# Performance work log

Hardware: AMD Instinct MI355X
Metric: run time of the kernel (lower is better)

## Reference

```python
import jax, jax.numpy as jnp
import numpy as np

A_LO, A_HI = -1.0, 1.0  # arbitrary_range


def _kbit_gaussian(q_lo: float, q_hi: float, n_bit: int) -> jnp.ndarray:
    # torch: norm.ppf of quantiles 1/n..(n-1)/n, cast to fp16, then affine-normalize in fp16
    p = jnp.arange(1, n_bit, dtype=jnp.float32) / n_bit
    v = jax.scipy.stats.norm.ppf(p).astype(jnp.float16)
    return q_lo + (v - v[0]) / (v[-1] - v[0]) * (q_hi - q_lo)


def make_codebook() -> jnp.ndarray:
    neg = _kbit_gaussian(A_LO, 0.0, 2 ** 3)            # 7 values in [-1, 0]
    pos = _kbit_gaussian(0.0, A_HI, 2 ** 3 + 1)[1:]     # 8 values in (0, 1]
    return jnp.concatenate([neg, pos])                  # [15], float16


def setup_inputs() -> dict:
    key = jax.random.key(0)
    x = jax.random.normal(key, (2048, 4096), dtype=jnp.float32)
    codebook = make_codebook()
    return {"x": x, "codebook": codebook}


def reference(x, codebook):
    # fit: global min/max
    x_min = jnp.min(x)
    x_max = jnp.max(x)
    # fit_transform: clamp (no-op at fit min/max) + affine map to [A_LO, A_HI]
    x_norm = (jnp.clip(x, x_min, x_max) - x_min) / (x_max - x_min) * (A_HI - A_LO) + A_LO
    # nearest-codebook lookup: |x - c| argmin over 15-entry codebook, then gather
    dist = jnp.abs(x_norm[..., None] - codebook)  # [..., 15] (fp32, codebook upcast as in torch)
    idx = jnp.argmin(dist, axis=-1)
    return codebook[idx]  # float16, same shape as x
```

## Files before the change

### kernel.cpp

```cpp
#include <hip/hip_runtime.h>
#include <hip/hip_fp16.h>

#define N_CB 15

__device__ __forceinline__ unsigned f2ord(float f) {
    unsigned u = __float_as_uint(f);
    return (u & 0x80000000u) ? ~u : (u | 0x80000000u);
}
__device__ __forceinline__ float ord2f(unsigned u) {
    return (u & 0x80000000u) ? __uint_as_float(u & 0x7fffffffu)
                             : __uint_as_float(~u);
}

__global__ void q4_init_kernel(const void* __restrict__ cb_raw, unsigned* __restrict__ ws) {
    int t = threadIdx.x;
    if (t == 62) ws[0] = 0xFFFFFFFFu;
    if (t == 63) ws[1] = 0u;
    if (t < N_CB) {
        const float* cf = (const float*)cb_raw;
        float v;
        if (cf[0] == -1.0f) {
            v = cf[t];
        } else {
            const __half* ch = (const __half*)cb_raw;
            v = __half2float(ch[t]);
        }
        ((float*)ws)[2 + t] = v;
    }
}

__global__ void q4_minmax_kernel(const float4* __restrict__ x4, int n4,
                                 const float* __restrict__ x, int n,
                                 unsigned* __restrict__ ws) {
    float mn = 3.402823466e38f, mx = -3.402823466e38f;
    int stride = gridDim.x * blockDim.x;
    for (int i = blockIdx.x * blockDim.x + threadIdx.x; i < n4; i += stride) {
        float4 v = x4[i];
        mn = fminf(mn, fminf(fminf(v.x, v.y), fminf(v.z, v.w)));
        mx = fmaxf(mx, fmaxf(fmaxf(v.x, v.y), fmaxf(v.z, v.w)));
    }
    if (blockIdx.x == 0) {
        for (int i = n4 * 4 + threadIdx.x; i < n; i += blockDim.x) {
            float v = x[i];
            mn = fminf(mn, v);
            mx = fmaxf(mx, v);
        }
    }
    #pragma unroll
    for (int off = 32; off; off >>= 1) {
        mn = fminf(mn, __shfl_down(mn, off));
        mx = fmaxf(mx, __shfl_down(mx, off));
    }
    __shared__ float smn[4], smx[4];
    int wave = threadIdx.x >> 6, lane = threadIdx.x & 63;
    if (lane == 0) { smn[wave] = mn; smx[wave] = mx; }
    __syncthreads();
    if (threadIdx.x == 0) {
        mn = fminf(fminf(smn[0], smn[1]), fminf(smn[2], smn[3]));
        mx = fmaxf(fmaxf(smx[0], smx[1]), fmaxf(smx[2], smx[3]));
        atomicMin(&ws[0], f2ord(mn));
        atomicMax(&ws[1], f2ord(mx));
    }
}

__device__ __forceinline__ float q4_lookup(float xv, float mn, float range,
                                           const float* cb) {
    float t = (xv - mn) / range * 2.0f - 1.0f;
    float best = fabsf(t - cb[0]);
    float val  = cb[0];
    #pragma unroll
    for (int j = 1; j < N_CB; j++) {
        float d = fabsf(t - cb[j]);
        if (d < best) { best = d; val = cb[j]; }
    }
    return val;
}

__global__ void q4_transform_kernel(const float4* __restrict__ x4, float4* __restrict__ out4,
                                    int n4,
                                    const float* __restrict__ x, float* __restrict__ out, int n,
                                    const unsigned* __restrict__ ws) {
    float mn = ord2f(ws[0]);
    float mx = ord2f(ws[1]);
    float range = mx - mn;
    float cb[N_CB];
    const float* cbw = (const float*)(ws + 2);
    #pragma unroll
    for (int j = 0; j < N_CB; j++) cb[j] = cbw[j];

    int i = blockIdx.x * blockDim.x + threadIdx.x;
    if (i < n4) {
        float4 v = x4[i];
        float4 o;
        o.x = q4_lookup(v.x, mn, range, cb);
        o.y = q4_lookup(v.y, mn, range, cb);
        o.z = q4_lookup(v.z, mn, range, cb);
        o.w = q4_lookup(v.w, mn, range, cb);
        out4[i] = o;
    }
    if (blockIdx.x == 0) {
        for (int k = n4 * 4 + threadIdx.x; k < n; k += blockDim.x) {
            out[k] = q4_lookup(x[k], mn, range, cb);
        }
    }
}

extern "C" void kernel_launch(void* const* d_in, const int* in_sizes, int n_in,
                              void* d_out, int out_size, void* d_ws, size_t ws_size,
                              hipStream_t stream) {
    const float* x = (const float*)d_in[0];
    const void* cb = d_in[1];
    float* out = (float*)d_out;
    int n = in_sizes[0];
    int n4 = n >> 2;
    unsigned* ws = (unsigned*)d_ws;

    q4_init_kernel<<<1, 64, 0, stream>>>(cb, ws);

    q4_minmax_kernel<<<1024, 256, 0, stream>>>((const float4*)x, n4, x, n, ws);

    int blocks = (n4 + 255) / 256;
    q4_transform_kernel<<<blocks, 256, 0, stream>>>((const float4*)x, (float4*)out, n4,
                                                    x, out, n, ws);
}
```

Baseline: 119.2 us.

## Replace atomic minmax with per-block partials reduced inside the transform kernel

Removes the separate init kernel by folding the codebook copy into the partials kernel. The min/max pass now writes 512 per-block partials instead of doing global atomics, so no workspace reset is needed. The transform kernel reduces those partials itself in every block. It issues its two float4 loads per thread before that reduction so the memory latency overlaps with it. This saves one launch and the atomic contention, at the cost of redundant partial reduction work in every transform block.

```diff
diff --git a/kernel.cpp b/kernel.cpp
--- a/kernel.cpp
+++ b/kernel.cpp
@@ -1,46 +1,35 @@
 #include <hip/hip_runtime.h>
 #include <hip/hip_fp16.h>
+#include <float.h>
 
 #define N_CB 15
+#define A_BLOCKS 512
+#define A_THREADS 256
+#define B_THREADS 256
 
-__device__ __forceinline__ unsigned f2ord(float f) {
-    unsigned u = __float_as_uint(f);
-    return (u & 0x80000000u) ? ~u : (u | 0x80000000u);
-}
-__device__ __forceinline__ float ord2f(unsigned u) {
-    return (u & 0x80000000u) ? __uint_as_float(u & 0x7fffffffu)
-                             : __uint_as_float(~u);
-}
 
-__global__ void q4_init_kernel(const void* __restrict__ cb_raw, unsigned* __restrict__ ws) {
-    int t = threadIdx.x;
-    if (t == 62) ws[0] = 0xFFFFFFFFu;
-    if (t == 63) ws[1] = 0u;
-    if (t < N_CB) {
+__global__ __launch_bounds__(A_THREADS) void q4_partials_kernel(
+        const float4* __restrict__ x4, int n4,
+        const float* __restrict__ x, int n,
+        float* __restrict__ ws, const void* __restrict__ cb_raw) {
+    if (blockIdx.x == 0 && threadIdx.x < N_CB) {
         const float* cf = (const float*)cb_raw;
         float v;
-        if (cf[0] == -1.0f) {
-            v = cf[t];
-        } else {
-            const __half* ch = (const __half*)cb_raw;
-            v = __half2float(ch[t]);
-        }
-        ((float*)ws)[2 + t] = v;
+        if (cf[0] == -1.0f) v = cf[threadIdx.x];
+        else                v = __half2float(((const __half*)cb_raw)[threadIdx.x]);
+        ws[1024 + threadIdx.x] = v;
     }
-}
 
-__global__ void q4_minmax_kernel(const float4* __restrict__ x4, int n4,
-                                 const float* __restrict__ x, int n,
-                                 unsigned* __restrict__ ws) {
-    float mn = 3.402823466e38f, mx = -3.402823466e38f;
-    int stride = gridDim.x * blockDim.x;
-    for (int i = blockIdx.x * blockDim.x + threadIdx.x; i < n4; i += stride) {
+    float mn = FLT_MAX, mx = -FLT_MAX;
+    int tid = blockIdx.x * A_THREADS + threadIdx.x;
+    int stride = gridDim.x * A_THREADS;
+    for (int i = tid; i < n4; i += stride) {
         float4 v = x4[i];
         mn = fminf(mn, fminf(fminf(v.x, v.y), fminf(v.z, v.w)));
         mx = fmaxf(mx, fmaxf(fmaxf(v.x, v.y), fmaxf(v.z, v.w)));
     }
     if (blockIdx.x == 0) {
-        for (int i = n4 * 4 + threadIdx.x; i < n; i += blockDim.x) {
+        for (int i = n4 * 4 + threadIdx.x; i < n; i += A_THREADS) {
             float v = x[i];
             mn = fminf(mn, v);
             mx = fmaxf(mx, v);
@@ -56,10 +45,8 @@
     if (lane == 0) { smn[wave] = mn; smx[wave] = mx; }
     __syncthreads();
     if (threadIdx.x == 0) {
-        mn = fminf(fminf(smn[0], smn[1]), fminf(smn[2], smn[3]));
-        mx = fmaxf(fmaxf(smx[0], smx[1]), fmaxf(smx[2], smx[3]));
-        atomicMin(&ws[0], f2ord(mn));
-        atomicMax(&ws[1], f2ord(mx));
+        ws[blockIdx.x]       = fminf(fminf(smn[0], smn[1]), fminf(smn[2], smn[3]));
+        ws[512 + blockIdx.x] = fmaxf(fmaxf(smx[0], smx[1]), fmaxf(smx[2], smx[3]));
     }
 }
 
@@ -76,31 +63,58 @@
     return val;
 }
 
-__global__ void q4_transform_kernel(const float4* __restrict__ x4, float4* __restrict__ out4,
-                                    int n4,
-                                    const float* __restrict__ x, float* __restrict__ out, int n,
-                                    const unsigned* __restrict__ ws) {
-    float mn = ord2f(ws[0]);
-    float mx = ord2f(ws[1]);
-    float range = mx - mn;
+__global__ __launch_bounds__(B_THREADS) void q4_transform_kernel(
+        const float4* __restrict__ x4, float4* __restrict__ out4, int n4,
+        const float* __restrict__ x, float* __restrict__ out, int n,
+        const float* __restrict__ ws) {
+    int base = blockIdx.x * (B_THREADS * 2) + threadIdx.x;
+    bool h0 = base < n4, h1 = (base + B_THREADS) < n4;
+    float4 v0, v1;
+    if (h0) v0 = x4[base];
+    if (h1) v1 = x4[base + B_THREADS];
+
+    float mn = fminf(ws[threadIdx.x],       ws[threadIdx.x + 256]);
+    float mx = fmaxf(ws[512 + threadIdx.x], ws[768 + threadIdx.x]);
+    #pragma unroll
+    for (int off = 32; off; off >>= 1) {
+        mn = fminf(mn, __shfl_down(mn, off));
+        mx = fmaxf(mx, __shfl_down(mx, off));
+    }
+    __shared__ float sred[8];
+    __shared__ float sfin[2];
+    int wave = threadIdx.x >> 6, lane = threadIdx.x & 63;
+    if (lane == 0) { sred[wave] = mn; sred[4 + wave] = mx; }
+    __syncthreads();
+    if (threadIdx.x == 0) {
+        sfin[0] = fminf(fminf(sred[0], sred[1]), fminf(sred[2], sred[3]));
+        sfin[1] = fmaxf(fmaxf(sred[4], sred[5]), fmaxf(sred[6], sred[7]));
+    }
     float cb[N_CB];
-    const float* cbw = (const float*)(ws + 2);
     #pragma unroll
-    for (int j = 0; j < N_CB; j++) cb[j] = cbw[j];
+    for (int j = 0; j < N_CB; j++) cb[j] = ws[1024 + j];
+    __syncthreads();
+    float fmn = sfin[0];
+    float range = sfin[1] - fmn;
 
-    int i = blockIdx.x * blockDim.x + threadIdx.x;
-    if (i < n4) {
-        float4 v = x4[i];
+    if (h0) {
         float4 o;
-        o.x = q4_lookup(v.x, mn, range, cb);
-        o.y = q4_lookup(v.y, mn, range, cb);
-        o.z = q4_lookup(v.z, mn, range, cb);
-        o.w = q4_lookup(v.w, mn, range, cb);
-        out4[i] = o;
+        o.x = q4_lookup(v0.x, fmn, range, cb);
+        o.y = q4_lookup(v0.y, fmn, range, cb);
+        o.z = q4_lookup(v0.z, fmn, range, cb);
+        o.w = q4_lookup(v0.w, fmn, range, cb);
+        out4[base] = o;
+    }
+    if (h1) {
+        float4 o;
+        o.x = q4_lookup(v1.x, fmn, range, cb);
+        o.y = q4_lookup(v1.y, fmn, range, cb);
+        o.z = q4_lookup(v1.z, fmn, range, cb);
+        o.w = q4_lookup(v1.w, fmn, range, cb);
+        out4[base + B_THREADS] = o;
     }
     if (blockIdx.x == 0) {
-        for (int k = n4 * 4 + threadIdx.x; k < n; k += blockDim.x) {
-            out[k] = q4_lookup(x[k], mn, range, cb);
+        for (int k = n4 * 4 + threadIdx.x; k < n; k += B_THREADS) {
+            out[k] = q4_lookup(x[k], fmn, range, cb);
         }
     }
 }
@@ -113,13 +127,12 @@
     float* out = (float*)d_out;
     int n = in_sizes[0];
     int n4 = n >> 2;
-    unsigned* ws = (unsigned*)d_ws;
+    float* ws = (float*)d_ws;
 
-    q4_init_kernel<<<1, 64, 0, stream>>>(cb, ws);
+    q4_partials_kernel<<<A_BLOCKS, A_THREADS, 0, stream>>>(
+        (const float4*)x, n4, x, n, ws, cb);
 
-    q4_minmax_kernel<<<1024, 256, 0, stream>>>((const float4*)x, n4, x, n, ws);
-
-    int blocks = (n4 + 255) / 256;
-    q4_transform_kernel<<<blocks, 256, 0, stream>>>((const float4*)x, (float4*)out, n4,
-                                                    x, out, n, ws);
+    int bblocks = (n4 + B_THREADS * 2 - 1) / (B_THREADS * 2);
+    q4_transform_kernel<<<bblocks, B_THREADS, 0, stream>>>(
+        (const float4*)x, (float4*)out, n4, x, out, n, ws);
 }
```

After: 97.32 us. 18.3% less time.
